# Kernel optimization log

Hardware: AMD Instinct MI355X
Metric: run time of the kernel (lower is better)

## Reference

```python
import jax, jax.numpy as jnp
import numpy as np

N, M = 100000, 12          # atoms, max neighbors
AF, NF = 64, 41            # atom_fea_len, nbr_fea_len
NC = 3                     # n_conv
N0, APC = 100, 1000        # crystals, atoms per crystal
HF, HID = 128, 64          # h_fea_len, hid_dim
EPS = 1e-5                 # batchnorm eps


def setup_inputs() -> dict:
    key = jax.random.key(0)
    ks = jax.random.split(key, 8)
    return dict(
        atom_num=jax.random.randint(ks[0], (N,), 0, 119),
        nbr_fea=jax.random.normal(ks[1], (N, M, NF), jnp.float32),
        nbr_fea_idx=jax.random.randint(ks[2], (N, M), 0, N),
        crystal_atom_idx=jnp.arange(N).reshape(N0, APC),
        embedding=jax.random.normal(ks[3], (119, AF), jnp.float32) * 0.1,
        W_full=jax.random.normal(ks[4], (NC, 2 * AF + NF, 2 * AF), jnp.float32) * 0.05,
        b_full=jnp.zeros((NC, 2 * AF), jnp.float32),
        bn1_g=jnp.ones((NC, 2 * AF), jnp.float32),
        bn1_b=jnp.zeros((NC, 2 * AF), jnp.float32),
        bn2_g=jnp.ones((NC, AF), jnp.float32),
        bn2_b=jnp.zeros((NC, AF), jnp.float32),
        W_fc=jax.random.normal(ks[5], (AF, HF), jnp.float32) * 0.05,
        b_fc=jnp.zeros((HF,), jnp.float32),
        W_out=jax.random.normal(ks[6], (HF, HID), jnp.float32) * 0.05,
        b_out=jnp.zeros((HID,), jnp.float32),
    )


def _batchnorm(x, g, b, axes):
    # training-mode BatchNorm1d: biased batch statistics over `axes`
    mu = jnp.mean(x, axes, keepdims=True)
    var = jnp.mean(jnp.square(x - mu), axes, keepdims=True)
    return (x - mu) * jax.lax.rsqrt(var + EPS) * g + b


def _conv_layer(atom_fea, nbr_fea, nbr_idx, Wf, bf, g1, b1, g2, b2):
    nbr_atom = atom_fea[nbr_idx]                                   # (N, M, AF) gather
    self_fea = jnp.broadcast_to(atom_fea[:, None, :], nbr_atom.shape)
    total = jnp.concatenate([self_fea, nbr_atom, nbr_fea], axis=2)  # (N, M, 2AF+NF)
    gated = total @ Wf + bf                                        # (N, M, 2AF)
    gated = _batchnorm(gated, g1, b1, (0, 1))                      # bn over N*M rows
    filt, core = jnp.split(gated, 2, axis=2)
    summed = jnp.sum(jax.nn.sigmoid(filt) * jax.nn.softplus(core), axis=1)  # (N, AF)
    summed = _batchnorm(summed, g2, b2, (0,))
    return jax.nn.softplus(atom_fea + summed)


def reference(atom_num, nbr_fea, nbr_fea_idx, crystal_atom_idx, embedding,
              W_full, b_full, bn1_g, bn1_b, bn2_g, bn2_b,
              W_fc, b_fc, W_out, b_out):
    atom_fea = embedding[atom_num]                                 # (N, AF)
    for i in range(NC):
        atom_fea = _conv_layer(atom_fea, nbr_fea, nbr_fea_idx,
                               W_full[i], b_full[i], bn1_g[i], bn1_b[i],
                               bn2_g[i], bn2_b[i])
    crys_fea = jnp.mean(atom_fea[crystal_atom_idx], axis=1)        # (N0, AF) pooling
    crys_fea = jax.nn.softplus(jax.nn.softplus(crys_fea) @ W_fc + b_fc)
    return crys_fea @ W_out + b_out                                # (N0, HID)
```

## Files before the change

kernel.cpp:

```cpp
#include <hip/hip_runtime.h>
#include <hip/hip_fp16.h>

#define N_ATOM 100000
#define M_NBR  12
#define NF     41
#define AF     64
#define NC     3
#define N0C    100
#define APC    1000
#define HF     128
#define HID    64
#define EPS    1e-5f
#define NTILE  75000

typedef unsigned short u16;
typedef unsigned int   u32;
typedef _Float16 half8 __attribute__((ext_vector_type(8)));
typedef float    f32x4 __attribute__((ext_vector_type(4)));

__device__ __forceinline__ float b2f(u16 u) {
    return __uint_as_float(((u32)u) << 16);
}
__device__ __forceinline__ u16 f2b(float f) {
    u32 x = __float_as_uint(f);
    u32 r = x + 0x7fffu + ((x >> 16) & 1u);
    return (u16)(r >> 16);
}
__device__ __forceinline__ float ldf(const void* p, long i, int f) {
    if (f) return ((const float*)p)[i];
    return b2f(((const u16*)p)[i]);
}
__device__ __forceinline__ float spf(float x) {
    return fmaxf(x, 0.0f) + __logf(1.0f + __expf(-fabsf(x)));
}
__device__ __forceinline__ float sigf(float x) {
    return __builtin_amdgcn_rcpf(1.0f + __expf(-x));
}
__device__ __forceinline__ float rdl(float v, int l) {
    return __uint_as_float((u32)__builtin_amdgcn_readlane(__float_as_uint(v), l));
}
__device__ __forceinline__ u32 packh2(float a, float b) {
    return (u32)__half_as_ushort(__float2half(a))
         | ((u32)__half_as_ushort(__float2half(b)) << 16);
}

__global__ void k_probe(const u16* __restrict__ nf, int* __restrict__ flag) {
    int t = threadIdx.x;
    int bad = 0;
    for (int i = t; i < 8192; i += 256) {
        u16 u = nf[i];
        float v = b2f(u);
        float a = fabsf(v);
        if (!(a <= 1024.0f) || (((u & 0x7fffu) != 0) && a < 1e-10f)) bad++;
    }
    __shared__ int cnt;
    if (t == 0) cnt = 0;
    __syncthreads();
    atomicAdd(&cnt, bad);
    __syncthreads();
    if (t == 0) flag[0] = (cnt > 800) ? 1 : 0;
}

__global__ void k_stage(const void* __restrict__ W, long Woff,
                        const void* __restrict__ b, long boff,
                        const void* __restrict__ g1, const void* __restrict__ b1,
                        const void* __restrict__ g2, const void* __restrict__ b2, long L,
                        float* __restrict__ Wst, float* __restrict__ bst,
                        float* __restrict__ bn1s, float* __restrict__ bn2s,
                        const int* __restrict__ flag) {
    int f = flag[0];
    long i = (long)blockIdx.x * 256 + threadIdx.x;
    const long NW_ = (long)(2 * AF + NF) * 128;
    if (i < NW_) {
        Wst[i] = ldf(W, Woff + i, f);
    } else if (i < NW_ + 128) {
        long c = i - NW_;
        bst[c] = ldf(b, boff + c, f);
        bn1s[c] = ldf(g1, L * 128 + c, f);
        bn1s[128 + c] = ldf(b1, L * 128 + c, f);
        if (c < 64) {
            bn2s[c] = ldf(g2, L * 64 + c, f);
            bn2s[64 + c] = ldf(b2, L * 64 + c, f);
        }
    }
}

__global__ void k_embed(const int* __restrict__ atom_num, const void* __restrict__ emb,
                        u16* __restrict__ af, const int* __restrict__ flag) {
    int f = flag[0];
    int i = blockIdx.x * 256 + threadIdx.x;
    if (i < N_ATOM * AF) {
        int n = i >> 6, c = i & 63;
        af[i] = f2b(ldf(emb, (long)atom_num[n] * AF + c, f));
    }
}

__global__ void k_nbrcvt(const void* __restrict__ nf, u32* __restrict__ Abuf,
                         const int* __restrict__ flag) {
    int f = flag[0];
    long d = (long)blockIdx.x * 256 + threadIdx.x;
    if (d >= (long)NTILE * 512) return;
    int tile = (int)(d >> 9);
    int rem  = (int)d & 511;
    int ks   = rem >> 8;
    int rem2 = rem & 255;
    int grp  = rem2 >> 6;
    int rem3 = rem2 & 63;
    int row  = rem3 >> 2;
    int kd   = rem3 & 3;
    int k0   = ks * 32 + grp * 8 + kd * 2;
    long e   = (long)tile * 16 + row;
    float v0 = (k0 < NF)     ? ldf(nf, e * NF + k0, f)     : 0.f;
    float v1 = (k0 + 1 < NF) ? ldf(nf, e * NF + k0 + 1, f) : 0.f;
    Abuf[d] = packh2(v0, v1);
}

__global__ __launch_bounds__(256) void k_an(const u16* __restrict__ af,
                       const float* __restrict__ Wst, u16* __restrict__ An) {
    int wv = threadIdx.x >> 6;
    int lane = threadIdx.x & 63;
    int n = blockIdx.x * 4 + wv;
    float afv = b2f(af[n * AF + lane]);
    float a0 = 0.f, a1 = 0.f;
    for (int k = 0; k < AF; ++k) {
        float a = __shfl(afv, k, 64);
        a0 = fmaf(a, Wst[(AF + k) * 128 + lane], a0);
        a1 = fmaf(a, Wst[(AF + k) * 128 + 64 + lane], a1);
    }
    An[(long)n * 128 + lane] = f2b(a0);
    An[(long)n * 128 + 64 + lane] = f2b(a1);
}

__global__ __launch_bounds__(256) void k_asn(const u16* __restrict__ af,
                       const float* __restrict__ Wst, const float* __restrict__ bst,
                       float* __restrict__ Rf, u16* __restrict__ Rh,
                       u16* __restrict__ An2, int rf) {
    int lane = threadIdx.x & 63;
    int n = blockIdx.x * 4 + (threadIdx.x >> 6);
    float afv = b2f(af[n * AF + lane]);
    float r0 = bst[lane], r1 = bst[64 + lane];
    float q0 = 0.f, q1 = 0.f;
    #pragma unroll 8
    for (int k = 0; k < AF; ++k) {
        float a = rdl(afv, k);
        r0 = fmaf(a, Wst[k * 128 + lane], r0);
        r1 = fmaf(a, Wst[k * 128 + 64 + lane], r1);
        q0 = fmaf(a, Wst[(AF + k) * 128 + lane], q0);
        q1 = fmaf(a, Wst[(AF + k) * 128 + 64 + lane], q1);
    }
    long p = (long)n * 64 + lane;
    if (rf) {
        *(float2*)(Rf + p * 2) = make_float2(r0, r1);
    } else {
        ((u32*)Rh)[p] = (u32)f2b(r0) | ((u32)f2b(r1) << 16);
    }
    ((u32*)An2)[p] = (u32)f2b(q0) | ((u32)f2b(q1) << 16);
}

__global__ __launch_bounds__(256) void k_gmfma(
        const u16* __restrict__ Abuf, const int* __restrict__ nbr_idx,
        const u16* __restrict__ An, const float* __restrict__ Wst,
        const float* __restrict__ Rf, u32* __restrict__ G,
        float* __restrict__ statsOut) {
    int lane = threadIdx.x & 63;
    int wv = threadIdx.x >> 6;
    int gw = blockIdx.x * 4 + wv;
    int NW = gridDim.x * 4;
    __shared__ u16 Blds[8192];
    __shared__ float red[256];
    for (int i = threadIdx.x; i < 8192; i += 256) {
        int ks = i >> 12;
        int r1 = i & 4095;
        int nt = r1 >> 9;
        int r2 = r1 & 511;
        int grp = r2 >> 7;
        int r3 = r2 & 127;
        int col = r3 >> 3;
        int ii = r3 & 7;
        int k = ks * 32 + grp * 8 + ii;
        float v = (k < NF) ? Wst[(128 + k) * 128 + nt * 16 + col] : 0.f;
        Blds[i] = __half_as_ushort(__float2half(v));
    }
    red[threadIdx.x] = 0.f;
    __syncthreads();

    const u32* An32 = (const u32*)An;
    const float2* R2 = (const float2*)Rf;
    int sub = ((lane >> 4) << 7) + ((lane & 15) << 3);
    float sL[4] = {0,0,0,0}, qL[4] = {0,0,0,0};
    float sH[4] = {0,0,0,0}, qH[4] = {0,0,0,0};

    for (int t = gw; t < NTILE; t += NW) {
        f32x4 acc[8];
        #pragma unroll
        for (int i = 0; i < 8; ++i) acc[i] = (f32x4){0.f, 0.f, 0.f, 0.f};
        const u16* Ab = Abuf + (size_t)t * 1024;
        #pragma unroll
        for (int ks = 0; ks < 2; ++ks) {
            half8 a = *(const half8*)(Ab + ks * 512 + sub);
            #pragma unroll
            for (int nt = 0; nt < 8; ++nt) {
                half8 b = *(const half8*)(Blds + ks * 4096 + nt * 512 + sub);
                acc[nt] = __builtin_amdgcn_mfma_f32_16x16x32_f16(a, b, acc[nt], 0, 0, 0);
            }
        }
        #pragma unroll
        for (int r = 0; r < 4; ++r) {
            int e = (t << 4) + ((lane >> 4) << 2) + r;
            int n = e / 12;
            int j = nbr_idx[e];
            #pragma unroll
            for (int np = 0; np < 4; ++np) {
                int c = (np << 4) + (lane & 15);
                float2 rv = R2[(size_t)n * 64 + c];
                u32 q = An32[(size_t)j * 64 + c];
                float g0 = acc[np][r] + rv.x + b2f((u16)(q & 0xffffu));
                float g1 = acc[np + 4][r] + rv.y + b2f((u16)(q >> 16));
                G[(size_t)e * 64 + c] = packh2(g0, g1);
                sL[np] += g0;  qL[np] += g0 * g0;
                sH[np] += g1;  qH[np] += g1 * g1;
            }
        }
    }
    __syncthreads();
    #pragma unroll
    for (int np = 0; np < 4; ++np) {
        int c = (np << 4) + (lane & 15);
        atomicAdd(&red[c], sL[np]);
        atomicAdd(&red[64 + c], sH[np]);
        atomicAdd(&red[128 + c], qL[np]);
        atomicAdd(&red[192 + c], qH[np]);
    }
    __syncthreads();
    atomicAdd(&statsOut[threadIdx.x], red[threadIdx.x]);
}

template<int GF>
__global__ __launch_bounds__(256) void k_gstat(const void* __restrict__ nbr_fea,
                       const int* __restrict__ nbr_idx,
                       const u16* __restrict__ An,
                       const float* __restrict__ Wst,
                       const float* __restrict__ Rf,
                       void* __restrict__ G,
                       float* __restrict__ statsOut,
                       const int* __restrict__ flag) {
    int f = flag[0];
    int lane = threadIdx.x & 63;
    int wv = threadIdx.x >> 6;
    int gwave = blockIdx.x * 4 + wv;
    int NW = gridDim.x * 4;
    __shared__ float2 wlds[NF][64];
    __shared__ float red[256];
    for (int i = threadIdx.x; i < NF * 64; i += 256) {
        int k = i >> 6, c = i & 63;
        wlds[k][c] = make_float2(Wst[(128 + k) * 128 + c],
                                 Wst[(128 + k) * 128 + 64 + c]);
    }
    __syncthreads();

    const u32* An32 = (const u32*)An;
    float sum0 = 0.f, ssq0 = 0.f, sum1 = 0.f, ssq1 = 0.f;

    for (int n = gwave; n < N_ATOM; n += NW) {
        float2 rr = *(const float2*)(Rf + ((long)n * 64 + lane) * 2);
        for (int mb = 0; mb < M_NBR; mb += 2) {
            long ra = (long)n * M_NBR + mb;
            int2 jj = *(const int2*)(nbr_idx + ra);
            float nv0, nv1;
            if (f) {
                const float* np = (const float*)nbr_fea + ra * NF;
                nv0 = (lane < NF) ? np[lane] : 0.f;
                nv1 = (lane < NF) ? np[NF + lane] : 0.f;
            } else {
                const u16* np = (const u16*)nbr_fea + ra * NF;
                nv0 = (lane < NF) ? b2f(np[lane]) : 0.f;
                nv1 = (lane < NF) ? b2f(np[NF + lane]) : 0.f;
            }
            u32 qa = An32[(long)jj.x * 64 + lane];
            u32 qb = An32[(long)jj.y * 64 + lane];
            float e00 = rr.x, e01 = rr.y, e10 = rr.x, e11 = rr.y;
            #pragma unroll
            for (int k = 0; k < NF; ++k) {
                float2 w = wlds[k][lane];
                float va = rdl(nv0, k);
                float vb = rdl(nv1, k);
                e00 = fmaf(va, w.x, e00);  e01 = fmaf(va, w.y, e01);
                e10 = fmaf(vb, w.x, e10);  e11 = fmaf(vb, w.y, e11);
            }
            float g00 = e00 + b2f((u16)(qa & 0xffffu));
            float g01 = e01 + b2f((u16)(qa >> 16));
            float g10 = e10 + b2f((u16)(qb & 0xffffu));
            float g11 = e11 + b2f((u16)(qb >> 16));
            if (GF) {
                float2* Gf = (float2*)G;
                Gf[(ra + 0) * 64 + lane] = make_float2(g00, g01);
                Gf[(ra + 1) * 64 + lane] = make_float2(g10, g11);
            } else {
                u32* Gh = (u32*)G;
                Gh[(ra + 0) * 64 + lane] = packh2(g00, g01);
                Gh[(ra + 1) * 64 + lane] = packh2(g10, g11);
            }
            sum0 += g00 + g10; ssq0 += g00 * g00 + g10 * g10;
            sum1 += g01 + g11; ssq1 += g01 * g01 + g11 * g11;
        }
    }

    red[threadIdx.x] = 0.f;
    __syncthreads();
    atomicAdd(&red[lane], sum0);
    atomicAdd(&red[64 + lane], sum1);
    atomicAdd(&red[128 + lane], ssq0);
    atomicAdd(&red[192 + lane], ssq1);
    __syncthreads();
    atomicAdd(&statsOut[threadIdx.x], red[threadIdx.x]);
}

template<int GF>
__global__ __launch_bounds__(256) void k_gapply(const void* __restrict__ G,
                       const float* __restrict__ st1,
                       u16* __restrict__ summed,
                       float* __restrict__ statsOut) {
    int lane = threadIdx.x & 63;
    int wv = threadIdx.x >> 6;
    int gwave = blockIdx.x * 4 + wv;
    int NW = gridDim.x * 4;
    float s0 = st1[lane],        s1 = st1[lane + 64];
    float t0 = st1[128 + lane],  t1 = st1[192 + lane];
    float sum0 = 0.f, ssq0 = 0.f;
    for (int n = gwave; n < N_ATOM; n += NW) {
        float asum = 0.f;
        long base = (long)n * M_NBR * 64 + lane;
        #pragma unroll
        for (int m = 0; m < M_NBR; ++m) {
            float g0, g1;
            if (GF) {
                float2 g = ((const float2*)G)[base + (long)m * 64];
                g0 = g.x; g1 = g.y;
            } else {
                u32 gp = ((const u32*)G)[base + (long)m * 64];
                g0 = __half2float(__ushort_as_half((u16)(gp & 0xffffu)));
                g1 = __half2float(__ushort_as_half((u16)(gp >> 16)));
            }
            asum += sigf(fmaf(g0, s0, t0)) * spf(fmaf(g1, s1, t1));
        }
        summed[(long)n * 64 + lane] = f2b(asum);
        sum0 += asum; ssq0 += asum * asum;
    }
    __shared__ float red[256];
    if (threadIdx.x < 128) red[threadIdx.x] = 0.f;
    __syncthreads();
    atomicAdd(&red[lane], sum0);
    atomicAdd(&red[64 + lane], ssq0);
    __syncthreads();
    if (threadIdx.x < 128) atomicAdd(&statsOut[threadIdx.x], red[threadIdx.x]);
}

template<bool APPLY, int MODE>
__global__ __launch_bounds__(256) void k_conv(const void* __restrict__ nbr_fea,
                       const int* __restrict__ nbr_idx,
                       const u16* __restrict__ af, const u16* __restrict__ An,
                       const float* __restrict__ Wst, const float* __restrict__ bst,
                       const float* __restrict__ st1,
                       u16* __restrict__ summed,
                       float* __restrict__ statsOut,
                       const int* __restrict__ flag,
                       const float* __restrict__ Rf, const u16* __restrict__ Rh, int rf) {
    int f = flag[0];
    int lane = threadIdx.x & 63;
    int wv = threadIdx.x >> 6;
    int gwave = blockIdx.x * 4 + wv;
    int NW = gridDim.x * 4;
    __shared__ float2 wlds[NF][64];
    __shared__ float red[256];

    float s0 = 0.f, t0 = 0.f, s1 = 0.f, t1 = 0.f;
    if (APPLY) {
        s0 = st1[lane];        s1 = st1[lane + 64];
        t0 = st1[128 + lane];  t1 = st1[192 + lane];
    }
    float sum0 = 0.f, ssq0 = 0.f, sum1 = 0.f, ssq1 = 0.f;

    if (MODE == 0) {
        for (int i = threadIdx.x; i < NF * 64; i += 256) {
            int k = i >> 6, c = i & 63;
            wlds[k][c] = make_float2(Wst[(128 + k) * 128 + c],
                                     Wst[(128 + k) * 128 + 64 + c]);
        }
        __syncthreads();

        for (int n = gwave; n < N_ATOM; n += NW) {
            long p = (long)n * 64 + lane;
            float r0, r1;
            if (rf) {
                float2 rr = *(const float2*)(Rf + p * 2);
                r0 = rr.x; r1 = rr.y;
            } else {
                u32 rr = ((const u32*)Rh)[p];
                r0 = b2f((u16)(rr & 0xffffu)); r1 = b2f((u16)(rr >> 16));
            }
            float asum = 0.f;
            for (int m = 0; m < M_NBR; m += 2) {
                long ra = (long)n * M_NBR + m;
                int2 jj = *(const int2*)(nbr_idx + ra);
                float nv0, nv1;
                if (f) {
                    const float* np = (const float*)nbr_fea + ra * NF;
                    nv0 = (lane < NF) ? np[lane] : 0.f;
                    nv1 = (lane < NF) ? np[NF + lane] : 0.f;
                } else {
                    const u16* np = (const u16*)nbr_fea + ra * NF;
                    nv0 = (lane < NF) ? b2f(np[lane]) : 0.f;
                    nv1 = (lane < NF) ? b2f(np[NF + lane]) : 0.f;
                }
                u32 qa = ((const u32*)An)[(long)jj.x * 64 + lane];
                u32 qb = ((const u32*)An)[(long)jj.y * 64 + lane];
                float ea0 = r0, ea1 = r1, eb0 = r0, eb1 = r1;
                #pragma unroll
                for (int k = 0; k < NF; ++k) {
                    float2 w = wlds[k][lane];
                    float va = rdl(nv0, k);
                    float vb = rdl(nv1, k);
                    ea0 = fmaf(va, w.x, ea0);
                    ea1 = fmaf(va, w.y, ea1);
                    eb0 = fmaf(vb, w.x, eb0);
                    eb1 = fmaf(vb, w.y, eb1);
                }
                float ga0 = ea0 + b2f((u16)(qa & 0xffffu));
                float ga1 = ea1 + b2f((u16)(qa >> 16));
                float gb0 = eb0 + b2f((u16)(qb & 0xffffu));
                float gb1 = eb1 + b2f((u16)(qb >> 16));
                if (APPLY) {
                    asum += sigf(fmaf(ga0, s0, t0)) * spf(fmaf(ga1, s1, t1));
                    asum += sigf(fmaf(gb0, s0, t0)) * spf(fmaf(gb1, s1, t1));
                } else {
                    sum0 += ga0 + gb0; ssq0 += ga0 * ga0 + gb0 * gb0;
                    sum1 += ga1 + gb1; ssq1 += ga1 * ga1 + gb1 * gb1;
                }
            }
            if (APPLY) {
                summed[p] = f2b(asum);
                sum0 += asum; ssq0 += asum * asum;
            }
        }
    } else {
        float w0[NF], w1[NF];
        #pragma unroll
        for (int k = 0; k < NF; ++k) {
            w0[k] = Wst[(128 + k) * 128 + lane];
            w1[k] = Wst[(128 + k) * 128 + 64 + lane];
        }
        float b0 = bst[lane];
        float b1 = bst[64 + lane];
        for (int n = gwave; n < N_ATOM; n += NW) {
            float afv = b2f(af[n * AF + lane]);
            float as0 = b0, as1 = b1;
            for (int k = 0; k < AF; ++k) {
                float a = __shfl(afv, k, 64);
                as0 = fmaf(a, Wst[k * 128 + lane], as0);
                as1 = fmaf(a, Wst[k * 128 + 64 + lane], as1);
            }
            float asum = 0.f;
            for (int m = 0; m < M_NBR; ++m) {
                long r = (long)n * M_NBR + m;
                int j = nbr_idx[r];
                float nv = (lane < NF) ? ldf(nbr_fea, r * NF + lane, f) : 0.f;
                float e0 = as0, e1 = as1;
                #pragma unroll
                for (int k = 0; k < NF; ++k) {
                    float v = __shfl(nv, k, 64);
                    e0 = fmaf(v, w0[k], e0);
                    e1 = fmaf(v, w1[k], e1);
                }
                float g0, g1;
                if (MODE == 2) {
                    float aj = b2f(af[(long)j * AF + lane]);
                    float an0 = 0.f, an1 = 0.f;
                    for (int k = 0; k < AF; ++k) {
                        float a = __shfl(aj, k, 64);
                        an0 = fmaf(a, Wst[(AF + k) * 128 + lane], an0);
                        an1 = fmaf(a, Wst[(AF + k) * 128 + 64 + lane], an1);
                    }
                    g0 = e0 + an0; g1 = e1 + an1;
                } else {
                    g0 = e0 + b2f(An[(long)j * 128 + lane]);
                    g1 = e1 + b2f(An[(long)j * 128 + 64 + lane]);
                }
                if (APPLY) {
                    float ft = sigf(fmaf(g0, s0, t0));
                    float cc = spf(fmaf(g1, s1, t1));
                    asum += ft * cc;
                } else {
                    sum0 += g0; ssq0 += g0 * g0;
                    sum1 += g1; ssq1 += g1 * g1;
                }
            }
            if (APPLY) {
                summed[(long)n * 64 + lane] = f2b(asum);
                sum0 += asum; ssq0 += asum * asum;
            }
        }
    }

    if (APPLY) {
        if (threadIdx.x < 128) red[threadIdx.x] = 0.f;
        __syncthreads();
        atomicAdd(&red[lane], sum0);
        atomicAdd(&red[64 + lane], ssq0);
        __syncthreads();
        if (threadIdx.x < 128) atomicAdd(&statsOut[threadIdx.x], red[threadIdx.x]);
    } else {
        red[threadIdx.x] = 0.f;
        __syncthreads();
        atomicAdd(&red[lane], sum0);
        atomicAdd(&red[64 + lane], sum1);
        atomicAdd(&red[128 + lane], ssq0);
        atomicAdd(&red[192 + lane], ssq1);
        __syncthreads();
        atomicAdd(&statsOut[threadIdx.x], red[threadIdx.x]);
    }
}

__global__ void k_bn1(const float* __restrict__ stats, const float* __restrict__ bn1s,
                      float* __restrict__ st) {
    int c = threadIdx.x;
    float cnt = (float)N_ATOM * (float)M_NBR;
    float mu = stats[c] / cnt;
    float var = fmaxf(stats[128 + c] / cnt - mu * mu, 0.0f);
    float s = bn1s[c] * rsqrtf(var + EPS);
    st[c] = s;
    st[128 + c] = bn1s[128 + c] - mu * s;
}

__global__ void k_bn2(const float* __restrict__ stats, const float* __restrict__ bn2s,
                      float* __restrict__ st) {
    int c = threadIdx.x;
    float cnt = (float)N_ATOM;
    float mu = stats[c] / cnt;
    float var = fmaxf(stats[64 + c] / cnt - mu * mu, 0.0f);
    float s = bn2s[c] * rsqrtf(var + EPS);
    st[c] = s;
    st[64 + c] = bn2s[64 + c] - mu * s;
}

__global__ void k_update(u16* __restrict__ af, const u16* __restrict__ summed,
                         const float* __restrict__ st2) {
    int i = blockIdx.x * 256 + threadIdx.x;
    if (i < N_ATOM * 64) {
        int c = i & 63;
        float v = fmaf(b2f(summed[i]), st2[c], st2[64 + c]);
        af[i] = f2b(spf(b2f(af[i]) + v));
    }
}

__global__ void k_pool(const u16* __restrict__ af, const int* __restrict__ cidx,
                       float* __restrict__ crysp) {
    int b = blockIdx.x;
    int ch = threadIdx.x & 63;
    int part = threadIdx.x >> 6;
    float acc = 0.f;
    for (int k = part; k < APC; k += 4) {
        int a = cidx[b * APC + k];
        acc += b2f(af[(long)a * 64 + ch]);
    }
    __shared__ float red[256];
    red[threadIdx.x] = acc;
    __syncthreads();
    if (part == 0) {
        float s = red[ch] + red[64 + ch] + red[128 + ch] + red[192 + ch];
        crysp[b * 64 + ch] = spf(s * (1.0f / APC));
    }
}

__global__ void k_head(const float* __restrict__ crysp, const void* __restrict__ Wfc,
                       const void* __restrict__ bfc, const void* __restrict__ Wout,
                       const void* __restrict__ bout, void* __restrict__ outv,
                       const int* __restrict__ flag) {
    int f = flag[0];
    int b = blockIdx.x;
    int t = threadIdx.x;
    __shared__ float cr[64];
    __shared__ float h[HF];
    if (t < 64) cr[t] = crysp[b * 64 + t];
    __syncthreads();
    float acc = ldf(bfc, t, f);
    for (int k = 0; k < 64; ++k) acc = fmaf(cr[k], ldf(Wfc, (long)k * HF + t, f), acc);
    h[t] = spf(acc);
    __syncthreads();
    if (t < HID) {
        float o = ldf(bout, t, f);
        for (int k = 0; k < HF; ++k) o = fmaf(h[k], ldf(Wout, (long)k * HID + t, f), o);
        if (f) ((float*)outv)[b * HID + t] = o;
        else   ((u16*)outv)[b * HID + t] = f2b(o);
    }
}

extern "C" void kernel_launch(void* const* d_in, const int* in_sizes, int n_in,
                              void* d_out, int out_size, void* d_ws, size_t ws_size,
                              hipStream_t stream) {
    const int* atom_num = (const int*)d_in[0];
    const void* nbr_fea = d_in[1];
    const int* nbr_idx  = (const int*)d_in[2];
    const int* cidx     = (const int*)d_in[3];
    const void* emb     = d_in[4];
    const void* W_full  = d_in[5];
    const void* b_full  = d_in[6];
    const void* bn1_g   = d_in[7];
    const void* bn1_b   = d_in[8];
    const void* bn2_g   = d_in[9];
    const void* bn2_b   = d_in[10];
    const void* W_fc    = d_in[11];
    const void* b_fc    = d_in[12];
    const void* W_out   = d_in[13];
    const void* b_out   = d_in[14];

    char* wsb = (char*)d_ws;
    int*   flag   = (int*)wsb;
    float* stats1 = (float*)(wsb + 16);
    float* st1    = stats1 + 256;
    float* stats2 = st1 + 256;
    float* st2    = stats2 + 128;
    float* crysp  = st2 + 128;
    float* Wst    = crysp + 6400;
    float* bst    = Wst + 21632;
    float* bn1s   = bst + 128;
    float* bn2s   = bn1s + 256;
    u16*   af     = (u16*)(bn2s + 128);
    u16*   summed = af + (long)N_ATOM * 64;
    u16*   An     = summed + (long)N_ATOM * 64;
    char*  afterAn = (char*)(An + (long)N_ATOM * 128);
    float* Rf = (float*)afterAn;
    u16*   Rh = (u16*)afterAn;
    char*  afterRf = afterAn + (size_t)N_ATOM * 128 * 4;
    void*  G = (void*)afterRf;

    size_t off_afterAn = (size_t)(afterAn - wsb);
    size_t need_f2  = off_afterAn + (size_t)N_ATOM * 128 * 4;
    size_t need_f2h = off_afterAn + (size_t)N_ATOM * 128 * 2;
    size_t need_f1  = off_afterAn;
    const size_t GBYTES32 = (size_t)N_ATOM * M_NBR * 128 * 4;
    const size_t GBYTES16 = (size_t)N_ATOM * M_NBR * 128 * 2;
    const size_t ABYTES   = (size_t)NTILE * 2048;
    u32* Abuf = (u32*)(afterRf + GBYTES16);
    size_t need_M  = need_f2 + GBYTES16 + ABYTES;
    size_t need_TA = need_f2 + GBYTES32;
    size_t need_TB = need_f2 + GBYTES16;
    int mf = (ws_size >= need_M) ? 1 : 0;
    int gf = (ws_size >= need_TA) ? 1 : ((ws_size >= need_TB) ? 0 : -1);
    int rf = (ws_size >= need_f2) ? 1 : ((ws_size >= need_f2h) ? 0 : -1);
    bool f1 = ws_size >= need_f1;

    k_probe<<<1, 256, 0, stream>>>((const u16*)nbr_fea, flag);
    if (mf) {
        k_nbrcvt<<<(int)(((long)NTILE * 512 + 255) / 256), 256, 0, stream>>>(
            nbr_fea, Abuf, flag);
    }
    k_embed<<<(N_ATOM * 64 + 255) / 256, 256, 0, stream>>>(atom_num, emb, af, flag);

    const long WROWS = (long)(2 * AF + NF) * 128;
    for (int L = 0; L < NC; ++L) {
        (void)hipMemsetAsync(stats1, 0, 768 * sizeof(float), stream);
        k_stage<<<(int)((WROWS + 128 + 255) / 256), 256, 0, stream>>>(
            W_full, (long)L * WROWS, b_full, (long)L * 128,
            bn1_g, bn1_b, bn2_g, bn2_b, (long)L,
            Wst, bst, bn1s, bn2s, flag);
        if (mf) {
            k_asn<<<N_ATOM / 4, 256, 0, stream>>>(af, Wst, bst, Rf, Rh, An, 1);
            k_gmfma<<<2500, 256, 0, stream>>>((const u16*)Abuf, nbr_idx, An, Wst,
                                              Rf, (u32*)G, stats1);
            k_bn1<<<1, 128, 0, stream>>>(stats1, bn1s, st1);
            k_gapply<0><<<2500, 256, 0, stream>>>(G, st1, summed, stats2);
        } else if (gf >= 0) {
            k_asn<<<N_ATOM / 4, 256, 0, stream>>>(af, Wst, bst, Rf, Rh, An, 1);
            if (gf == 1)
                k_gstat<1><<<2500, 256, 0, stream>>>(nbr_fea, nbr_idx, An, Wst, Rf,
                                                     G, stats1, flag);
            else
                k_gstat<0><<<2500, 256, 0, stream>>>(nbr_fea, nbr_idx, An, Wst, Rf,
                                                     G, stats1, flag);
            k_bn1<<<1, 128, 0, stream>>>(stats1, bn1s, st1);
            if (gf == 1)
                k_gapply<1><<<2500, 256, 0, stream>>>(G, st1, summed, stats2);
            else
                k_gapply<0><<<2500, 256, 0, stream>>>(G, st1, summed, stats2);
        } else if (rf >= 0) {
            k_asn<<<N_ATOM / 4, 256, 0, stream>>>(af, Wst, bst, Rf, Rh, An, rf);
            k_conv<false, 0><<<2500, 256, 0, stream>>>(nbr_fea, nbr_idx, af, An,
                Wst, bst, nullptr, nullptr, stats1, flag, Rf, Rh, rf);
            k_bn1<<<1, 128, 0, stream>>>(stats1, bn1s, st1);
            k_conv<true, 0><<<2500, 256, 0, stream>>>(nbr_fea, nbr_idx, af, An,
                Wst, bst, st1, summed, stats2, flag, Rf, Rh, rf);
        } else if (f1) {
            k_an<<<N_ATOM / 4, 256, 0, stream>>>(af, Wst, An);
            k_conv<false, 1><<<2500, 256, 0, stream>>>(nbr_fea, nbr_idx, af, An,
                Wst, bst, nullptr, nullptr, stats1, flag, nullptr, nullptr, 0);
            k_bn1<<<1, 128, 0, stream>>>(stats1, bn1s, st1);
            k_conv<true, 1><<<2500, 256, 0, stream>>>(nbr_fea, nbr_idx, af, An,
                Wst, bst, st1, summed, stats2, flag, nullptr, nullptr, 0);
        } else {
            k_conv<false, 2><<<2500, 256, 0, stream>>>(nbr_fea, nbr_idx, af, nullptr,
                Wst, bst, nullptr, nullptr, stats1, flag, nullptr, nullptr, 0);
            k_bn1<<<1, 128, 0, stream>>>(stats1, bn1s, st1);
            k_conv<true, 2><<<2500, 256, 0, stream>>>(nbr_fea, nbr_idx, af, nullptr,
                Wst, bst, st1, summed, stats2, flag, nullptr, nullptr, 0);
        }
        k_bn2<<<1, 64, 0, stream>>>(stats2, bn2s, st2);
        k_update<<<(N_ATOM * 64 + 255) / 256, 256, 0, stream>>>(af, summed, st2);
    }
    k_pool<<<N0C, 256, 0, stream>>>(af, cidx, crysp);
    k_head<<<N0C, HF, 0, stream>>>(crysp, W_fc, b_fc, W_out, b_out, d_out, flag);
}
```

Measured before the change: 2.164 ms.

## Recompute gated MFMA tiles in second pass instead of storing intermediate G

The statistics pass no longer writes the large per-edge gated tensor G. A new kernel recomputes the MFMA tiles and neighbor gathers, applies the batchnorm affine, sigmoid and softplus, and reduces over the 12 neighbors, working on groups of three 16-edge tiles so that four atoms line up with wave lane groups. This trades a write and a re-read of a large fp16 buffer for repeated MFMA and gather work.

```diff
diff --git a/kernel.cpp b/kernel.cpp
--- a/kernel.cpp
+++ b/kernel.cpp
@@ -12,6 +12,7 @@
 #define HID    64
 #define EPS    1e-5f
 #define NTILE  75000
+#define NSUP   25000
 
 typedef unsigned short u16;
 typedef unsigned int   u32;
@@ -38,6 +39,9 @@
 }
 __device__ __forceinline__ float rdl(float v, int l) {
     return __uint_as_float((u32)__builtin_amdgcn_readlane(__float_as_uint(v), l));
+}
+__device__ __forceinline__ float shflf(float v, int src) {
+    return __shfl(v, src, 64);
 }
 __device__ __forceinline__ u32 packh2(float a, float b) {
     return (u32)__half_as_ushort(__float2half(a))
@@ -157,17 +161,7 @@
     ((u32*)An2)[p] = (u32)f2b(q0) | ((u32)f2b(q1) << 16);
 }
 
-__global__ __launch_bounds__(256) void k_gmfma(
-        const u16* __restrict__ Abuf, const int* __restrict__ nbr_idx,
-        const u16* __restrict__ An, const float* __restrict__ Wst,
-        const float* __restrict__ Rf, u32* __restrict__ G,
-        float* __restrict__ statsOut) {
-    int lane = threadIdx.x & 63;
-    int wv = threadIdx.x >> 6;
-    int gw = blockIdx.x * 4 + wv;
-    int NW = gridDim.x * 4;
-    __shared__ u16 Blds[8192];
-    __shared__ float red[256];
+__device__ __forceinline__ void stage_blds(u16* Blds, const float* __restrict__ Wst) {
     for (int i = threadIdx.x; i < 8192; i += 256) {
         int ks = i >> 12;
         int r1 = i & 4095;
@@ -181,6 +175,20 @@
         float v = (k < NF) ? Wst[(128 + k) * 128 + nt * 16 + col] : 0.f;
         Blds[i] = __half_as_ushort(__float2half(v));
     }
+}
+
+__global__ __launch_bounds__(256) void k_gmfma(
+        const u16* __restrict__ Abuf, const int* __restrict__ nbr_idx,
+        const u16* __restrict__ An, const float* __restrict__ Wst,
+        const float* __restrict__ Rf,
+        float* __restrict__ statsOut) {
+    int lane = threadIdx.x & 63;
+    int wv = threadIdx.x >> 6;
+    int gw = blockIdx.x * 4 + wv;
+    int NW = gridDim.x * 4;
+    __shared__ u16 Blds[8192];
+    __shared__ float red[256];
+    stage_blds(Blds, Wst);
     red[threadIdx.x] = 0.f;
     __syncthreads();
 
@@ -216,7 +224,6 @@
                 u32 q = An32[(size_t)j * 64 + c];
                 float g0 = acc[np][r] + rv.x + b2f((u16)(q & 0xffffu));
                 float g1 = acc[np + 4][r] + rv.y + b2f((u16)(q >> 16));
-                G[(size_t)e * 64 + c] = packh2(g0, g1);
                 sL[np] += g0;  qL[np] += g0 * g0;
                 sH[np] += g1;  qH[np] += g1 * g1;
             }
@@ -233,6 +240,98 @@
     }
     __syncthreads();
     atomicAdd(&statsOut[threadIdx.x], red[threadIdx.x]);
+}
+
+#define TILE_BODY(PART, TT)                                                    \
+  {                                                                            \
+    int t = 3 * s + TT;                                                        \
+    f32x4 acc[8];                                                              \
+    _Pragma("unroll") for (int i = 0; i < 8; ++i)                              \
+        acc[i] = (f32x4){0.f, 0.f, 0.f, 0.f};                                  \
+    const u16* Ab = Abuf + (size_t)t * 1024;                                   \
+    _Pragma("unroll") for (int ks = 0; ks < 2; ++ks) {                         \
+      half8 a = *(const half8*)(Ab + ks * 512 + sub);                          \
+      _Pragma("unroll") for (int nt = 0; nt < 8; ++nt) {                       \
+        half8 b = *(const half8*)(Blds + ks * 4096 + nt * 512 + sub);          \
+        acc[nt] = __builtin_amdgcn_mfma_f32_16x16x32_f16(a, b, acc[nt],0,0,0); \
+      }                                                                        \
+    }                                                                          \
+    _Pragma("unroll") for (int r = 0; r < 4; ++r) {                            \
+      int e = (t << 4) + (grp << 2) + r;                                       \
+      int n = e / 12;                                                          \
+      int j = nbr_idx[e];                                                      \
+      _Pragma("unroll") for (int np = 0; np < 4; ++np) {                       \
+        int c = (np << 4) + cl;                                                \
+        float2 rv = R2[(size_t)n * 64 + c];                                    \
+        u32 q = An32[(size_t)j * 64 + c];                                      \
+        float g0 = acc[np][r] + rv.x + b2f((u16)(q & 0xffffu));                \
+        float g1 = acc[np + 4][r] + rv.y + b2f((u16)(q >> 16));                \
+        PART[np] += sigf(fmaf(g0, s0v[np], t0v[np]))                           \
+                  * spf(fmaf(g1, s1v[np], t1v[np]));                           \
+      }                                                                        \
+    }                                                                          \
+  }
+
+__global__ __launch_bounds__(256) void k_gvsum(
+        const u16* __restrict__ Abuf, const int* __restrict__ nbr_idx,
+        const u16* __restrict__ An, const float* __restrict__ Wst,
+        const float* __restrict__ Rf, const float* __restrict__ st1,
+        u16* __restrict__ summed, float* __restrict__ statsOut) {
+    int lane = threadIdx.x & 63;
+    int cl = lane & 15;
+    int grp = lane >> 4;
+    int wv = threadIdx.x >> 6;
+    int gw = blockIdx.x * 4 + wv;
+    int NW = gridDim.x * 4;
+    __shared__ u16 Blds[8192];
+    __shared__ float red[256];
+    stage_blds(Blds, Wst);
+    red[threadIdx.x] = 0.f;
+    __syncthreads();
+
+    const u32* An32 = (const u32*)An;
+    const float2* R2 = (const float2*)Rf;
+    int sub = (grp << 7) + (cl << 3);
+    float s0v[4], s1v[4], t0v[4], t1v[4];
+    #pragma unroll
+    for (int np = 0; np < 4; ++np) {
+        int c = (np << 4) + cl;
+        s0v[np] = st1[c];        s1v[np] = st1[64 + c];
+        t0v[np] = st1[128 + c];  t1v[np] = st1[192 + c];
+    }
+    float sB[4] = {0,0,0,0}, qB[4] = {0,0,0,0};
+
+    for (int s = gw; s < NSUP; s += NW) {
+        float p0[4] = {0,0,0,0}, p1[4] = {0,0,0,0}, p2[4] = {0,0,0,0};
+        TILE_BODY(p0, 0)
+        TILE_BODY(p1, 1)
+        TILE_BODY(p2, 2)
+        #pragma unroll
+        for (int np = 0; np < 4; ++np) {
+            float v00 = shflf(p0[np], cl),      v01 = shflf(p0[np], 16 + cl);
+            float v02 = shflf(p0[np], 32 + cl), v03 = shflf(p0[np], 48 + cl);
+            float v10 = shflf(p1[np], cl),      v11 = shflf(p1[np], 16 + cl);
+            float v12 = shflf(p1[np], 32 + cl), v13 = shflf(p1[np], 48 + cl);
+            float v20 = shflf(p2[np], cl),      v21 = shflf(p2[np], 16 + cl);
+            float v22 = shflf(p2[np], 32 + cl), v23 = shflf(p2[np], 48 + cl);
+            float asum = (grp == 0) ? (v00 + v01 + v02)
+                       : (grp == 1) ? (v03 + v10 + v11)
+                       : (grp == 2) ? (v12 + v13 + v20)
+                                    : (v21 + v22 + v23);
+            summed[(size_t)(4 * s + grp) * 64 + (np << 4) + cl] = f2b(asum);
+            sB[np] += asum;
+            qB[np] += asum * asum;
+        }
+    }
+    __syncthreads();
+    #pragma unroll
+    for (int np = 0; np < 4; ++np) {
+        int c = (np << 4) + cl;
+        atomicAdd(&red[c], sB[np]);
+        atomicAdd(&red[64 + c], qB[np]);
+    }
+    __syncthreads();
+    if (threadIdx.x < 128) atomicAdd(&statsOut[threadIdx.x], red[threadIdx.x]);
 }
 
 template<int GF>
@@ -666,9 +765,10 @@
         if (mf) {
             k_asn<<<N_ATOM / 4, 256, 0, stream>>>(af, Wst, bst, Rf, Rh, An, 1);
             k_gmfma<<<2500, 256, 0, stream>>>((const u16*)Abuf, nbr_idx, An, Wst,
-                                              Rf, (u32*)G, stats1);
+                                              Rf, stats1);
             k_bn1<<<1, 128, 0, stream>>>(stats1, bn1s, st1);
-            k_gapply<0><<<2500, 256, 0, stream>>>(G, st1, summed, stats2);
+            k_gvsum<<<2500, 256, 0, stream>>>((const u16*)Abuf, nbr_idx, An, Wst,
+                                              Rf, st1, summed, stats2);
         } else if (gf >= 0) {
             k_asn<<<N_ATOM / 4, 256, 0, stream>>>(af, Wst, bst, Rf, Rh, An, 1);
             if (gf == 1)
```

Result: slower. 2.413 ms (+11.5%).
